# Performance work log

Hardware: AMD Instinct MI355X
Metric: run time of the kernel (lower is better)

Reference implementation:

```python
import jax, jax.numpy as jnp
import numpy as np

WIN = 32  # window_size


def _groupnorm(x, w, b, eps=1e-5):
    # GroupNorm(1, dim): normalize over (C, W, H) per sample, per-channel affine
    mu = x.mean(axis=(1, 2, 3), keepdims=True)
    var = x.var(axis=(1, 2, 3), keepdims=True)
    xh = (x - mu) * jax.lax.rsqrt(var + eps)
    return xh * w[None, :, None, None] + b[None, :, None, None]


def setup_inputs() -> dict:
    key = jax.random.key(0)
    ks = jax.random.split(key, 7)
    B, C, W, H = 2, 1, 64, 1024
    d = 32
    x = jax.random.normal(ks[0], (B, C, W, H), jnp.float32)
    # 1x1 convs == per-pixel linear maps; store weights as [out, in]
    w_in = jax.random.normal(ks[1], (d, C), jnp.float32) * 0.5
    w_q = jax.random.normal(ks[2], (d, d), jnp.float32) * d ** -0.5
    w_k = jax.random.normal(ks[3], (d, d), jnp.float32) * d ** -0.5
    w_v = jax.random.normal(ks[4], (d, d), jnp.float32) * d ** -0.5
    w_out = jax.random.normal(ks[5], (C, d), jnp.float32) * d ** -0.5
    gn_w = jnp.ones((d,), jnp.float32)
    gn_b = jnp.zeros((d,), jnp.float32)
    gamma = jnp.array(1.0, jnp.float32)
    return {"x": x, "w_in": w_in, "w_q": w_q, "w_k": w_k, "w_v": w_v,
            "w_out": w_out, "gn_w": gn_w, "gn_b": gn_b, "gamma": gamma}


def reference(x, w_in, w_q, w_k, w_v, w_out, gn_w, gn_b, gamma):
    B, C, W, H = x.shape
    d = w_in.shape[0]
    scale = d ** -0.5

    feat = jnp.einsum('bcwh,dc->bdwh', x, w_in)              # in_proj (1x1 conv)
    z = jax.nn.gelu(_groupnorm(feat, gn_w, gn_b), approximate=False)
    q = jnp.einsum('bdwh,ed->bewh', z, w_q)
    k = jnp.einsum('bdwh,ed->bewh', z, w_k)
    v = jnp.einsum('bdwh,ed->bewh', z, w_v)

    def rows(t):  # [B,d,W,H] -> [B*W, H, d]
        return t.transpose(0, 2, 3, 1).reshape(B * W, H, d)

    q, k, v = rows(q), rows(k), rows(v)

    attn = jnp.einsum('nid,njd->nij', q * scale, k)          # [N, H, H]
    idx = jnp.arange(H)
    band = jnp.abs(idx[None, :] - idx[:, None]) <= WIN       # True = visible
    attn = jnp.where(band[None], attn, jnp.finfo(attn.dtype).min)
    attn = jax.nn.softmax(attn, axis=-1)

    o = jnp.einsum('nij,njd->nid', attn, v)                  # [N, H, d]
    o = o.reshape(B, W, H, d).transpose(0, 3, 1, 2)          # [B, d, W, H]

    out = feat + gamma * o
    out = jax.nn.gelu(_groupnorm(out, gn_w, gn_b), approximate=False)
    return jnp.einsum('bdwh,cd->bcwh', out, w_out)           # out_proj
```

## Files before the change

### kernel.cpp

```cpp
#include <hip/hip_runtime.h>
#include <hip/hip_bf16.h>
#include <cmath>

#define H_DIM 1024
#define W_DIM 64
#define N_BATCH 2
#define DCH 32
#define WINR 32
#define TQ 256
#define HALO (TQ + 2*WINR)
#define NROW (N_BATCH * W_DIM)

__device__ __forceinline__ float gelu_f(float v) {
    return 0.5f * v * (1.0f + erff(v * 0.70710678118654752440f));
}

__global__ void k_init(double* __restrict__ acc) {
    int t = threadIdx.x;
    if (t < 8) acc[t] = 0.0;
}

__global__ __launch_bounds__(256) void k_xstats(const float* __restrict__ x,
                                                double* __restrict__ acc) {
    const int b = blockIdx.x;
    const int t = threadIdx.x;
    float4 v = ((const float4*)(x + (size_t)b * 1024))[t];
    double s  = (double)v.x + (double)v.y + (double)v.z + (double)v.w;
    double s2 = (double)v.x*(double)v.x + (double)v.y*(double)v.y +
                (double)v.z*(double)v.z + (double)v.w*(double)v.w;
    #pragma unroll
    for (int o = 32; o; o >>= 1) {
        s  += __shfl_down(s, o);
        s2 += __shfl_down(s2, o);
    }
    if ((t & 63) == 0) {
        const int batch = b >> 6;
        atomicAdd(&acc[batch*2 + 0], s);
        atomicAdd(&acc[batch*2 + 1], s2);
    }
}

__global__ __launch_bounds__(256) void k_main(
    const float* __restrict__ x,
    const float* __restrict__ w_in,
    const float* __restrict__ w_q,
    const float* __restrict__ w_k,
    const float* __restrict__ w_v,
    const float* __restrict__ gn_w,
    const float* __restrict__ gn_b,
    const float* __restrict__ gammap,
    const double* __restrict__ stats,
    double* __restrict__ gn2acc,
    float* __restrict__ out_pre)
{
    __shared__ float zs[HALO * DCH];
    __shared__ float ks[HALO * DCH];
    __shared__ float vs[HALO * DCH];

    const int t    = threadIdx.x;
    const int bid  = blockIdx.x;
    const int row  = bid >> 2;
    const int tile = bid & 3;
    const int batch = row >> 6;
    const int h0 = tile * TQ;
    const int g0 = h0 - WINR;

    const double Sx  = stats[batch*2 + 0];
    const double Sx2 = stats[batch*2 + 1];
    float sw = 0.f, sw2 = 0.f;
    #pragma unroll
    for (int d = 0; d < DCH; ++d) { float w = w_in[d]; sw += w; sw2 += w*w; }
    const double n1   = (double)DCH * W_DIM * H_DIM;
    const double mu1d = (double)sw  * Sx  / n1;
    const double ex2  = (double)sw2 * Sx2 / n1;
    const double var1 = ex2 - mu1d*mu1d;
    const float mu1   = (float)mu1d;
    const float rstd1 = (float)(1.0 / sqrt(var1 + 1e-5));

    const float* xrow = x + (size_t)row * H_DIM;

    #pragma unroll 4
    for (int rep = 0; rep < (HALO * DCH) / 256; ++rep) {
        int idx = rep * 256 + t;
        int p = idx >> 5;
        int d = idx & 31;
        int h = g0 + p;
        float xv = ((unsigned)h < H_DIM) ? xrow[h] : 0.f;
        float feat = xv * w_in[d];
        float zv = gelu_f((feat - mu1) * rstd1 * gn_w[d] + gn_b[d]);
        int cp = (d >> 2) ^ (p & 7);
        zs[p * DCH + cp * 4 + (d & 3)] = zv;
    }
    __syncthreads();

    const int e  = t & 31;
    const int pg = t >> 5;
    float4 wkr[8], wvr[8];
    #pragma unroll
    for (int c = 0; c < 8; ++c) {
        wkr[c] = ((const float4*)(w_k + e * DCH))[c];
        wvr[c] = ((const float4*)(w_v + e * DCH))[c];
    }
    #pragma unroll 4
    for (int pass = 0; pass < HALO / 8; ++pass) {
        int p = pass * 8 + pg;
        float ka = 0.f, va = 0.f;
        #pragma unroll
        for (int c = 0; c < 8; ++c) {
            float4 z4 = ((const float4*)zs)[p * 8 + (c ^ pg)];
            ka += z4.x*wkr[c].x + z4.y*wkr[c].y + z4.z*wkr[c].z + z4.w*wkr[c].w;
            va += z4.x*wvr[c].x + z4.y*wvr[c].y + z4.z*wvr[c].z + z4.w*wvr[c].w;
        }
        int cp = (e >> 2) ^ pg;
        ks[p * DCH + cp * 4 + (e & 3)] = ka;
        vs[p * DCH + cp * 4 + (e & 3)] = va;
    }

    float4 z4r[8];
    {
        int p = t + WINR;
        int pm = p & 7;
        #pragma unroll
        for (int c = 0; c < 8; ++c)
            z4r[c] = ((const float4*)zs)[p * 8 + (c ^ pm)];
    }
    float q[DCH];
    #pragma unroll
    for (int e2 = 0; e2 < DCH; ++e2) {
        const float4* wq4 = (const float4*)(w_q + e2 * DCH);
        float acc = 0.f;
        #pragma unroll
        for (int c = 0; c < 8; ++c) {
            float4 wv4 = wq4[c];
            acc += z4r[c].x*wv4.x + z4r[c].y*wv4.y + z4r[c].z*wv4.z + z4r[c].w*wv4.w;
        }
        q[e2] = acc * 0.17677669529663688f;
    }
    __syncthreads();

    float m = -3.0e38f, l = 0.f;
    float o[DCH];
    #pragma unroll
    for (int d = 0; d < DCH; ++d) o[d] = 0.f;

    const int hq = h0 + t;
    #pragma unroll 2
    for (int off = 0; off <= 2 * WINR; ++off) {
        int p = t + off;
        int j = g0 + p;
        int pm = p & 7;
        bool valid = ((unsigned)j < H_DIM);
        float acc = 0.f;
        #pragma unroll
        for (int c = 0; c < 8; ++c) {
            float4 k4 = ((const float4*)ks)[p * 8 + (c ^ pm)];
            acc += q[4*c+0]*k4.x + q[4*c+1]*k4.y + q[4*c+2]*k4.z + q[4*c+3]*k4.w;
        }
        float mn   = valid ? fmaxf(m, acc) : m;
        float corr = __expf(m - mn);
        float pw   = valid ? __expf(acc - mn) : 0.f;
        l = l * corr + pw;
        m = mn;
        #pragma unroll
        for (int c = 0; c < 8; ++c) {
            float4 v4 = ((const float4*)vs)[p * 8 + (c ^ pm)];
            o[4*c+0] = o[4*c+0]*corr + pw*v4.x;
            o[4*c+1] = o[4*c+1]*corr + pw*v4.y;
            o[4*c+2] = o[4*c+2]*corr + pw*v4.z;
            o[4*c+3] = o[4*c+3]*corr + pw*v4.w;
        }
    }
    const float inv = 1.0f / l;

    const float xq = xrow[hq];
    const float gamma = gammap[0];
    float so = 0.f, so2 = 0.f;
    float* op = out_pre + ((size_t)row * H_DIM + hq) * DCH;
    #pragma unroll
    for (int c = 0; c < 8; ++c) {
        float4 wi4 = ((const float4*)w_in)[c];
        float4 r;
        r.x = xq * wi4.x + gamma * (o[4*c+0] * inv);
        r.y = xq * wi4.y + gamma * (o[4*c+1] * inv);
        r.z = xq * wi4.z + gamma * (o[4*c+2] * inv);
        r.w = xq * wi4.w + gamma * (o[4*c+3] * inv);
        ((float4*)op)[c] = r;
        so  += r.x + r.y + r.z + r.w;
        so2 += r.x*r.x + r.y*r.y + r.z*r.z + r.w*r.w;
    }
    double ds = (double)so, ds2 = (double)so2;
    #pragma unroll
    for (int ofs = 32; ofs; ofs >>= 1) {
        ds  += __shfl_down(ds, ofs);
        ds2 += __shfl_down(ds2, ofs);
    }
    if ((t & 63) == 0) {
        atomicAdd(&gn2acc[batch*2 + 0], ds);
        atomicAdd(&gn2acc[batch*2 + 1], ds2);
    }
}

__global__ __launch_bounds__(256) void k_out(
    const float* __restrict__ out_pre,
    const float* __restrict__ w_out,
    const float* __restrict__ gn_w,
    const float* __restrict__ gn_b,
    const double* __restrict__ acc,
    float* __restrict__ outp)
{
    const int pix = blockIdx.x * 256 + threadIdx.x;
    const int batch = pix >> 16;
    const double n2 = 2097152.0;
    const double S  = acc[4 + batch*2];
    const double S2 = acc[5 + batch*2];
    const double mu = S / n2;
    const double var = S2 / n2 - mu * mu;
    const float muf  = (float)mu;
    const float rstd = (float)(1.0 / sqrt(var + 1e-5));

    const float4* ip = (const float4*)(out_pre + (size_t)pix * DCH);
    float acc_o = 0.f;
    #pragma unroll
    for (int c = 0; c < 8; ++c) {
        float4 v  = ip[c];
        float4 gw = ((const float4*)gn_w)[c];
        float4 gb = ((const float4*)gn_b)[c];
        float4 wo = ((const float4*)w_out)[c];
        acc_o += gelu_f((v.x - muf) * rstd * gw.x + gb.x) * wo.x;
        acc_o += gelu_f((v.y - muf) * rstd * gw.y + gb.y) * wo.y;
        acc_o += gelu_f((v.z - muf) * rstd * gw.z + gb.z) * wo.z;
        acc_o += gelu_f((v.w - muf) * rstd * gw.w + gb.w) * wo.w;
    }
    outp[pix] = acc_o;
}

extern "C" void kernel_launch(void* const* d_in, const int* in_sizes, int n_in,
                              void* d_out, int out_size, void* d_ws, size_t ws_size,
                              hipStream_t stream) {
    const float* x     = (const float*)d_in[0];
    const float* w_in  = (const float*)d_in[1];
    const float* w_q   = (const float*)d_in[2];
    const float* w_k   = (const float*)d_in[3];
    const float* w_v   = (const float*)d_in[4];
    const float* w_out = (const float*)d_in[5];
    const float* gn_w  = (const float*)d_in[6];
    const float* gn_b  = (const float*)d_in[7];
    const float* gamma = (const float*)d_in[8];

    double* acc    = (double*)d_ws;
    float* out_pre = (float*)((char*)d_ws + 256);
    float* outp    = (float*)d_out;

    k_init  <<<dim3(1),   dim3(64),  0, stream>>>(acc);
    k_xstats<<<dim3(128), dim3(256), 0, stream>>>(x, acc);
    k_main  <<<dim3(NROW * (H_DIM / TQ)), dim3(256), 0, stream>>>(
        x, w_in, w_q, w_k, w_v, gn_w, gn_b, gamma, acc, acc + 4, out_pre);
    k_out   <<<dim3(512), dim3(256), 0, stream>>>(out_pre, w_out, gn_w, gn_b, acc, outp);
}
```

Baseline: 234.0 us.

## Restructure banded attention with per-thread projections, wave-uniform tiles, lazy rescale, deterministic reductions

The zs shared buffer is removed. Each thread now computes its own z, K, V and Q rows in registers, with a precomputed affine folded into the GELU input. The attention loop iterates over a wave-shared 128-key window per 64-lane wave, so key and value loads become broadcast LDS reads. Online-softmax rescaling is applied only when some lane's max grows by more than 8. Atomic-based statistics are replaced by per-block partial sums reduced in later kernels, which drops the init kernel. The trade-off is roughly double the score computations per query and higher register pressure under the launch_bounds occupancy hint.

```diff
diff --git a/kernel.cpp b/kernel.cpp
--- a/kernel.cpp
+++ b/kernel.cpp
@@ -1,46 +1,67 @@
 #include <hip/hip_runtime.h>
-#include <hip/hip_bf16.h>
 #include <cmath>
 
 #define H_DIM 1024
-#define W_DIM 64
-#define N_BATCH 2
 #define DCH 32
 #define WINR 32
 #define TQ 256
 #define HALO (TQ + 2*WINR)
-#define NROW (N_BATCH * W_DIM)
+#define NBLK 512
 
 __device__ __forceinline__ float gelu_f(float v) {
     return 0.5f * v * (1.0f + erff(v * 0.70710678118654752440f));
 }
 
-__global__ void k_init(double* __restrict__ acc) {
-    int t = threadIdx.x;
-    if (t < 8) acc[t] = 0.0;
+__device__ __forceinline__ int swz(int p, int c) { return p * 8 + (c ^ (p & 7)); }
+
+__device__ __forceinline__ void matvec32(const float* __restrict__ w,
+                                         const float zv[DCH], float out[DCH]) {
+    #pragma unroll
+    for (int e = 0; e < DCH; ++e) {
+        const float* wr = w + e * DCH;
+        float a0 = 0.f, a1 = 0.f, a2 = 0.f, a3 = 0.f;
+        #pragma unroll
+        for (int d = 0; d < DCH; d += 4) {
+            a0 = fmaf(zv[d+0], wr[d+0], a0);
+            a1 = fmaf(zv[d+1], wr[d+1], a1);
+            a2 = fmaf(zv[d+2], wr[d+2], a2);
+            a3 = fmaf(zv[d+3], wr[d+3], a3);
+        }
+        out[e] = (a0 + a1) + (a2 + a3);
+    }
+}
+
+__device__ __forceinline__ void write_row(float* buf, int p, const float r[DCH]) {
+    #pragma unroll
+    for (int c = 0; c < 8; ++c)
+        ((float4*)buf)[swz(p, c)] =
+            make_float4(r[4*c+0], r[4*c+1], r[4*c+2], r[4*c+3]);
 }
 
 __global__ __launch_bounds__(256) void k_xstats(const float* __restrict__ x,
-                                                double* __restrict__ acc) {
+                                                double* __restrict__ part) {
+    __shared__ double red[8];
     const int b = blockIdx.x;
     const int t = threadIdx.x;
-    float4 v = ((const float4*)(x + (size_t)b * 1024))[t];
-    double s  = (double)v.x + (double)v.y + (double)v.z + (double)v.w;
-    double s2 = (double)v.x*(double)v.x + (double)v.y*(double)v.y +
-                (double)v.z*(double)v.z + (double)v.w*(double)v.w;
-    #pragma unroll
-    for (int o = 32; o; o >>= 1) {
-        s  += __shfl_down(s, o);
-        s2 += __shfl_down(s2, o);
-    }
-    if ((t & 63) == 0) {
-        const int batch = b >> 6;
-        atomicAdd(&acc[batch*2 + 0], s);
-        atomicAdd(&acc[batch*2 + 1], s2);
-    }
-}
-
-__global__ __launch_bounds__(256) void k_main(
+    const float4* px = (const float4*)(x + (size_t)b * 8192);
+    double s = 0.0, s2 = 0.0;
+    #pragma unroll
+    for (int i = 0; i < 8; ++i) {
+        float4 v = px[i * 256 + t];
+        s  += (double)v.x + (double)v.y + (double)v.z + (double)v.w;
+        s2 += (double)v.x*v.x + (double)v.y*v.y + (double)v.z*v.z + (double)v.w*v.w;
+    }
+    #pragma unroll
+    for (int o = 32; o; o >>= 1) { s += __shfl_down(s, o); s2 += __shfl_down(s2, o); }
+    if ((t & 63) == 0) { red[(t>>6)*2] = s; red[(t>>6)*2+1] = s2; }
+    __syncthreads();
+    if (t == 0) {
+        part[b*2+0] = red[0]+red[2]+red[4]+red[6];
+        part[b*2+1] = red[1]+red[3]+red[5]+red[7];
+    }
+}
+
+__global__ __launch_bounds__(256, 2) void k_main(
     const float* __restrict__ x,
     const float* __restrict__ w_in,
     const float* __restrict__ w_q,
@@ -49,141 +70,135 @@
     const float* __restrict__ gn_w,
     const float* __restrict__ gn_b,
     const float* __restrict__ gammap,
-    const double* __restrict__ stats,
-    double* __restrict__ gn2acc,
+    const double* __restrict__ xpart,
+    double* __restrict__ gn2part,
     float* __restrict__ out_pre)
 {
-    __shared__ float zs[HALO * DCH];
     __shared__ float ks[HALO * DCH];
     __shared__ float vs[HALO * DCH];
 
-    const int t    = threadIdx.x;
-    const int bid  = blockIdx.x;
-    const int row  = bid >> 2;
-    const int tile = bid & 3;
+    const int t     = threadIdx.x;
+    const int bid   = blockIdx.x;
+    const int row   = bid >> 2;
+    const int tile  = bid & 3;
     const int batch = row >> 6;
-    const int h0 = tile * TQ;
-    const int g0 = h0 - WINR;
-
-    const double Sx  = stats[batch*2 + 0];
-    const double Sx2 = stats[batch*2 + 1];
+    const int h0    = tile * TQ;
+    const int g0    = h0 - WINR;
+
+    double Sx = 0.0, Sx2 = 0.0;
+    const double* bp = xpart + batch * 16;
+    #pragma unroll
+    for (int i = 0; i < 8; ++i) { Sx += bp[2*i]; Sx2 += bp[2*i+1]; }
     float sw = 0.f, sw2 = 0.f;
     #pragma unroll
     for (int d = 0; d < DCH; ++d) { float w = w_in[d]; sw += w; sw2 += w*w; }
-    const double n1   = (double)DCH * W_DIM * H_DIM;
-    const double mu1d = (double)sw  * Sx  / n1;
-    const double ex2  = (double)sw2 * Sx2 / n1;
-    const double var1 = ex2 - mu1d*mu1d;
-    const float mu1   = (float)mu1d;
-    const float rstd1 = (float)(1.0 / sqrt(var1 + 1e-5));
+    const double n1   = 2097152.0;
+    const double mu1d = (double)sw * Sx / n1;
+    const double var1 = (double)sw2 * Sx2 / n1 - mu1d * mu1d;
+    const float  mu1  = (float)mu1d;
+    const float  rstd1 = (float)(1.0 / sqrt(var1 + 1e-5));
+
+    float ca[DCH], cb[DCH];
+    #pragma unroll
+    for (int d = 0; d < DCH; ++d) {
+        float a = rstd1 * gn_w[d];
+        ca[d] = w_in[d] * a;
+        cb[d] = gn_b[d] - mu1 * a;
+    }
 
     const float* xrow = x + (size_t)row * H_DIM;
 
-    #pragma unroll 4
-    for (int rep = 0; rep < (HALO * DCH) / 256; ++rep) {
-        int idx = rep * 256 + t;
-        int p = idx >> 5;
-        int d = idx & 31;
-        int h = g0 + p;
-        float xv = ((unsigned)h < H_DIM) ? xrow[h] : 0.f;
-        float feat = xv * w_in[d];
-        float zv = gelu_f((feat - mu1) * rstd1 * gn_w[d] + gn_b[d]);
-        int cp = (d >> 2) ^ (p & 7);
-        zs[p * DCH + cp * 4 + (d & 3)] = zv;
-    }
-    __syncthreads();
-
-    const int e  = t & 31;
-    const int pg = t >> 5;
-    float4 wkr[8], wvr[8];
-    #pragma unroll
-    for (int c = 0; c < 8; ++c) {
-        wkr[c] = ((const float4*)(w_k + e * DCH))[c];
-        wvr[c] = ((const float4*)(w_v + e * DCH))[c];
-    }
-    #pragma unroll 4
-    for (int pass = 0; pass < HALO / 8; ++pass) {
-        int p = pass * 8 + pg;
-        float ka = 0.f, va = 0.f;
-        #pragma unroll
-        for (int c = 0; c < 8; ++c) {
-            float4 z4 = ((const float4*)zs)[p * 8 + (c ^ pg)];
-            ka += z4.x*wkr[c].x + z4.y*wkr[c].y + z4.z*wkr[c].z + z4.w*wkr[c].w;
-            va += z4.x*wvr[c].x + z4.y*wvr[c].y + z4.z*wvr[c].z + z4.w*wvr[c].w;
-        }
-        int cp = (e >> 2) ^ pg;
-        ks[p * DCH + cp * 4 + (e & 3)] = ka;
-        vs[p * DCH + cp * 4 + (e & 3)] = va;
-    }
-
-    float4 z4r[8];
+    const float xq = xrow[h0 + t];
+    float q[DCH];
     {
-        int p = t + WINR;
-        int pm = p & 7;
-        #pragma unroll
-        for (int c = 0; c < 8; ++c)
-            z4r[c] = ((const float4*)zs)[p * 8 + (c ^ pm)];
-    }
-    float q[DCH];
-    #pragma unroll
-    for (int e2 = 0; e2 < DCH; ++e2) {
-        const float4* wq4 = (const float4*)(w_q + e2 * DCH);
-        float acc = 0.f;
-        #pragma unroll
-        for (int c = 0; c < 8; ++c) {
-            float4 wv4 = wq4[c];
-            acc += z4r[c].x*wv4.x + z4r[c].y*wv4.y + z4r[c].z*wv4.z + z4r[c].w*wv4.w;
-        }
-        q[e2] = acc * 0.17677669529663688f;
-    }
-    __syncthreads();
+        float zv[DCH];
+        #pragma unroll
+        for (int d = 0; d < DCH; ++d) zv[d] = gelu_f(fmaf(xq, ca[d], cb[d]));
+        float kr[DCH], vr[DCH];
+        matvec32(w_k, zv, kr);
+        matvec32(w_v, zv, vr);
+        write_row(ks, t + WINR, kr);
+        write_row(vs, t + WINR, vr);
+        matvec32(w_q, zv, q);
+        #pragma unroll
+        for (int e = 0; e < DCH; ++e) q[e] *= 0.17677669529663688f;
+    }
+    if (t < 64) {
+        const int p0 = (t < 32) ? t : (256 + t);
+        const int h  = g0 + p0;
+        const float xv = ((unsigned)h < H_DIM) ? xrow[h] : 0.f;
+        float zv[DCH];
+        #pragma unroll
+        for (int d = 0; d < DCH; ++d) zv[d] = gelu_f(fmaf(xv, ca[d], cb[d]));
+        float kr[DCH], vr[DCH];
+        matvec32(w_k, zv, kr);
+        matvec32(w_v, zv, vr);
+        write_row(ks, p0, kr);
+        write_row(vs, p0, vr);
+    }
+    __syncthreads();
+
+    const int lane  = t & 63;
+    const int wid   = t >> 6;
+    const int pbase = wid * 64;
+    const int jbase = g0 + pbase;
 
     float m = -3.0e38f, l = 0.f;
     float o[DCH];
     #pragma unroll
     for (int d = 0; d < DCH; ++d) o[d] = 0.f;
 
-    const int hq = h0 + t;
     #pragma unroll 2
-    for (int off = 0; off <= 2 * WINR; ++off) {
-        int p = t + off;
-        int j = g0 + p;
-        int pm = p & 7;
-        bool valid = ((unsigned)j < H_DIM);
-        float acc = 0.f;
+    for (int kk = 0; kk < 128; ++kk) {
+        const int p  = pbase + kk;
+        const int pm = p & 7;
+        const float4* kb = (const float4*)ks + p * 8;
+        float a0 = 0.f, a1 = 0.f, a2 = 0.f, a3 = 0.f;
         #pragma unroll
         for (int c = 0; c < 8; ++c) {
-            float4 k4 = ((const float4*)ks)[p * 8 + (c ^ pm)];
-            acc += q[4*c+0]*k4.x + q[4*c+1]*k4.y + q[4*c+2]*k4.z + q[4*c+3]*k4.w;
-        }
-        float mn   = valid ? fmaxf(m, acc) : m;
-        float corr = __expf(m - mn);
-        float pw   = valid ? __expf(acc - mn) : 0.f;
-        l = l * corr + pw;
-        m = mn;
+            float4 k4 = kb[c ^ pm];
+            a0 = fmaf(q[4*c+0], k4.x, a0);
+            a1 = fmaf(q[4*c+1], k4.y, a1);
+            a2 = fmaf(q[4*c+2], k4.z, a2);
+            a3 = fmaf(q[4*c+3], k4.w, a3);
+        }
+        const float s = (a0 + a1) + (a2 + a3);
+        const bool valid = ((unsigned)(kk - lane) <= 64u) &&
+                           ((unsigned)(jbase + kk) < (unsigned)H_DIM);
+        const float se = valid ? s : -3.0e38f;
+        if (__any(se > m + 8.0f)) {
+            const float mn = fmaxf(m, se);
+            const float corr = __expf(m - mn);
+            l *= corr;
+            #pragma unroll
+            for (int d = 0; d < DCH; ++d) o[d] *= corr;
+            m = mn;
+        }
+        const float pw = valid ? __expf(se - m) : 0.f;
+        l += pw;
+        const float4* vb = (const float4*)vs + p * 8;
         #pragma unroll
         for (int c = 0; c < 8; ++c) {
-            float4 v4 = ((const float4*)vs)[p * 8 + (c ^ pm)];
-            o[4*c+0] = o[4*c+0]*corr + pw*v4.x;
-            o[4*c+1] = o[4*c+1]*corr + pw*v4.y;
-            o[4*c+2] = o[4*c+2]*corr + pw*v4.z;
-            o[4*c+3] = o[4*c+3]*corr + pw*v4.w;
+            float4 v4 = vb[c ^ pm];
+            o[4*c+0] = fmaf(pw, v4.x, o[4*c+0]);
+            o[4*c+1] = fmaf(pw, v4.y, o[4*c+1]);
+            o[4*c+2] = fmaf(pw, v4.z, o[4*c+2]);
+            o[4*c+3] = fmaf(pw, v4.w, o[4*c+3]);
         }
     }
     const float inv = 1.0f / l;
 
-    const float xq = xrow[hq];
     const float gamma = gammap[0];
     float so = 0.f, so2 = 0.f;
-    float* op = out_pre + ((size_t)row * H_DIM + hq) * DCH;
+    float* op = out_pre + ((size_t)row * H_DIM + (h0 + t)) * DCH;
     #pragma unroll
     for (int c = 0; c < 8; ++c) {
         float4 wi4 = ((const float4*)w_in)[c];
         float4 r;
-        r.x = xq * wi4.x + gamma * (o[4*c+0] * inv);
-        r.y = xq * wi4.y + gamma * (o[4*c+1] * inv);
-        r.z = xq * wi4.z + gamma * (o[4*c+2] * inv);
-        r.w = xq * wi4.w + gamma * (o[4*c+3] * inv);
+        r.x = fmaf(gamma, o[4*c+0] * inv, xq * wi4.x);
+        r.y = fmaf(gamma, o[4*c+1] * inv, xq * wi4.y);
+        r.z = fmaf(gamma, o[4*c+2] * inv, xq * wi4.z);
+        r.w = fmaf(gamma, o[4*c+3] * inv, xq * wi4.w);
         ((float4*)op)[c] = r;
         so  += r.x + r.y + r.z + r.w;
         so2 += r.x*r.x + r.y*r.y + r.z*r.z + r.w*r.w;
@@ -194,9 +209,13 @@
         ds  += __shfl_down(ds, ofs);
         ds2 += __shfl_down(ds2, ofs);
     }
-    if ((t & 63) == 0) {
-        atomicAdd(&gn2acc[batch*2 + 0], ds);
-        atomicAdd(&gn2acc[batch*2 + 1], ds2);
+    __syncthreads();
+    double* red = (double*)ks;
+    if (lane == 0) { red[wid*2] = ds; red[wid*2+1] = ds2; }
+    __syncthreads();
+    if (t == 0) {
+        gn2part[bid*2+0] = red[0]+red[2]+red[4]+red[6];
+        gn2part[bid*2+1] = red[1]+red[3]+red[5]+red[7];
     }
 }
 
@@ -205,19 +224,32 @@
     const float* __restrict__ w_out,
     const float* __restrict__ gn_w,
     const float* __restrict__ gn_b,
-    const double* __restrict__ acc,
+    const double* __restrict__ gn2part,
     float* __restrict__ outp)
 {
-    const int pix = blockIdx.x * 256 + threadIdx.x;
-    const int batch = pix >> 16;
+    __shared__ double red[8];
+    const int t   = threadIdx.x;
+    const int bid = blockIdx.x;
+    const int batch = bid >> 8;
+
+    const double* gp = gn2part + (size_t)batch * 512;
+    double ds = gp[2*t], ds2 = gp[2*t+1];
+    #pragma unroll
+    for (int ofs = 32; ofs; ofs >>= 1) {
+        ds  += __shfl_down(ds, ofs);
+        ds2 += __shfl_down(ds2, ofs);
+    }
+    if ((t & 63) == 0) { red[(t>>6)*2] = ds; red[(t>>6)*2+1] = ds2; }
+    __syncthreads();
+    const double S  = red[0]+red[2]+red[4]+red[6];
+    const double S2 = red[1]+red[3]+red[5]+red[7];
     const double n2 = 2097152.0;
-    const double S  = acc[4 + batch*2];
-    const double S2 = acc[5 + batch*2];
     const double mu = S / n2;
     const double var = S2 / n2 - mu * mu;
     const float muf  = (float)mu;
     const float rstd = (float)(1.0 / sqrt(var + 1e-5));
 
+    const int pix = bid * 256 + t;
     const float4* ip = (const float4*)(out_pre + (size_t)pix * DCH);
     float acc_o = 0.f;
     #pragma unroll
@@ -247,13 +279,13 @@
     const float* gn_b  = (const float*)d_in[7];
     const float* gamma = (const float*)d_in[8];
 
-    double* acc    = (double*)d_ws;
-    float* out_pre = (float*)((char*)d_ws + 256);
-    float* outp    = (float*)d_out;
-
-    k_init  <<<dim3(1),   dim3(64),  0, stream>>>(acc);
-    k_xstats<<<dim3(128), dim3(256), 0, stream>>>(x, acc);
-    k_main  <<<dim3(NROW * (H_DIM / TQ)), dim3(256), 0, stream>>>(
-        x, w_in, w_q, w_k, w_v, gn_w, gn_b, gamma, acc, acc + 4, out_pre);
-    k_out   <<<dim3(512), dim3(256), 0, stream>>>(out_pre, w_out, gn_w, gn_b, acc, outp);
-}
+    double* xpart   = (double*)d_ws;
+    double* gn2part = (double*)((char*)d_ws + 256);
+    float*  out_pre = (float*)((char*)d_ws + 8448);
+    float*  outp    = (float*)d_out;
+
+    k_xstats<<<dim3(16),   dim3(256), 0, stream>>>(x, xpart);
+    k_main  <<<dim3(NBLK), dim3(256), 0, stream>>>(
+        x, w_in, w_q, w_k, w_v, gn_w, gn_b, gamma, xpart, gn2part, out_pre);
+    k_out   <<<dim3(512),  dim3(256), 0, stream>>>(out_pre, w_out, gn_w, gn_b, gn2part, outp);
+}
```

Result: slower. 309.1 us (+32.1%).
